# Performance work log

Hardware: AMD Instinct MI355X
Metric: run time of the kernel (lower is better)

## Reference

```python
import jax, jax.numpy as jnp
import numpy as np

D_MODEL = 512
N_HEADS = 8
D_HEAD = D_MODEL // N_HEADS
SCALE = 1.0 / np.sqrt(D_MODEL).astype(np.float32)  # source divides by sqrt(d_model), not sqrt(d_head)


def setup_inputs() -> dict:
    key = jax.random.key(0)
    ks = jax.random.split(key, 9)
    B, S = 4, 2048
    std = 1.0 / np.sqrt(D_MODEL).astype(np.float32)
    x = jax.random.normal(ks[0], (B, S, D_MODEL), dtype=jnp.float32)
    Wq = jax.random.normal(ks[1], (D_MODEL, D_MODEL), dtype=jnp.float32) * std
    bq = jnp.zeros((D_MODEL,), jnp.float32)
    Wk = jax.random.normal(ks[2], (D_MODEL, D_MODEL), dtype=jnp.float32) * std
    bk = jnp.zeros((D_MODEL,), jnp.float32)
    Wv = jax.random.normal(ks[3], (D_MODEL, D_MODEL), dtype=jnp.float32) * std
    bv = jnp.zeros((D_MODEL,), jnp.float32)
    Wo = jax.random.normal(ks[4], (D_MODEL, D_MODEL), dtype=jnp.float32) * std
    bo = jnp.zeros((D_MODEL,), jnp.float32)
    return {"x": x, "Wq": Wq, "bq": bq, "Wk": Wk, "bk": bk,
            "Wv": Wv, "bv": bv, "Wo": Wo, "bo": bo}


def reference(x, Wq, bq, Wk, bk, Wv, bv, Wo, bo):
    B, S, _ = x.shape
    # projections -> [B, H, S, Dh]
    def split_heads(t):
        return t.reshape(B, S, N_HEADS, D_HEAD).transpose(0, 2, 1, 3)
    q = split_heads(x @ Wq + bq)
    k = split_heads(x @ Wk + bk)
    v = split_heads(x @ Wv + bv)
    # scores: [B, H, S, S], scaled by 1/sqrt(d_model) as in source
    scores = jnp.einsum('bhqd,bhkd->bhqk', q, k) * SCALE
    weights = jax.nn.softmax(scores, axis=-1)
    # dropout is identity at inference time
    att = jnp.einsum('bhqk,bhkd->bhqd', weights, v)
    att = att.transpose(0, 2, 1, 3).reshape(B, S, D_MODEL)
    return att @ Wo + bo
```

## Files before the change

kernel.cpp:

```cpp
#include <hip/hip_runtime.h>
#include <math.h>

#define BATCH   4
#define S_LEN   2048
#define DMODEL  512
#define NHEADS  8
#define DHEAD   64
#define M_TOT   8192
#define ATT_SCALE 0.04419417382415922f
#define QSCALE (ATT_SCALE * 1.44269504088896f)

using short8  = __attribute__((ext_vector_type(8))) short;
using short4v = __attribute__((ext_vector_type(4))) short;
using floatx4 = __attribute__((ext_vector_type(4))) float;

__device__ __forceinline__ ushort f2bf(float f) {
    union { float f; unsigned u; } x; x.f = f;
    unsigned u = x.u + 0x7FFFu + ((x.u >> 16) & 1u);
    return (ushort)(u >> 16);
}
__device__ __forceinline__ unsigned pk2(float a, float b) {
    return (unsigned)f2bf(a) | ((unsigned)f2bf(b) << 16);
}
__device__ __forceinline__ unsigned pkr2(float a, float b) {
    unsigned ua = __float_as_uint(a) + 0x8000u;
    unsigned ub = __float_as_uint(b) + 0x8000u;
    return __builtin_amdgcn_perm(ub, ua, 0x07060302u);
}

__global__ __launch_bounds__(256) void prep(
    const float* __restrict__ x,
    const float* __restrict__ Wq, const float* __restrict__ Wk,
    const float* __restrict__ Wv, const float* __restrict__ Wo,
    ushort* __restrict__ xb, ushort* __restrict__ WT)
{
    const int bid = blockIdx.x;
    if (bid < 4096) {
        const int i = (bid * 256 + threadIdx.x) * 4;
        float4 f = *(const float4*)(x + i);
        uint2 o; o.x = pk2(f.x, f.y); o.y = pk2(f.z, f.w);
        *(uint2*)(xb + i) = o;
    } else {
        const int rb = bid - 4096;
        const int p  = rb >> 6;
        const int rem = rb & 63;
        const int n  = (rem >> 5) * 256 + threadIdx.x;
        const int k0 = (rem & 31) * 16;
        const float* W = (p == 0) ? Wq : (p == 1) ? Wk : (p == 2) ? Wv : Wo;
        unsigned u[8];
        #pragma unroll
        for (int j = 0; j < 8; ++j) {
            float a = W[(k0 + 2 * j)     * DMODEL + n];
            float b = W[(k0 + 2 * j + 1) * DMODEL + n];
            u[j] = pk2(a, b);
        }
        ushort* dst = WT + ((size_t)p * DMODEL + n) * DMODEL + k0;
        *(uint4*)dst       = *(uint4*)&u[0];
        *(uint4*)(dst + 8) = *(uint4*)&u[4];
    }
}

__global__ __launch_bounds__(256, 4) void qkv_gemm(
    const ushort* __restrict__ xb, const ushort* __restrict__ WT,
    const float* __restrict__ bq, const float* __restrict__ bk, const float* __restrict__ bv,
    ushort* __restrict__ q, ushort* __restrict__ k, ushort* __restrict__ vT)
{
    __shared__ ushort SMEM[128 * 136];
    ushort (*A)[40] = (ushort(*)[40])SMEM;
    ushort (*B)[40] = (ushort(*)[40])(SMEM + 128 * 40);
    ushort (*CT)[136] = (ushort(*)[136])SMEM;

    const int tid = threadIdx.x;
    const int wv  = tid >> 6, lane = tid & 63, l16 = lane & 15, quad = lane >> 4;
    const int m0  = blockIdx.x * 128;
    const int ng0 = blockIdx.y * 128;
    const int p   = ng0 >> 9;
    const int n0  = ng0 & 511;
    const ushort* Wp  = WT + (size_t)p * DMODEL * DMODEL + (size_t)n0 * DMODEL;
    const float* bias = (p == 0) ? bq : (p == 1) ? bk : bv;
    const float scl   = (p == 0) ? QSCALE : 1.0f;

    const int wm = (wv & 1) * 64, wn = (wv >> 1) * 64;
    floatx4 acc[4][4] = {};
    const int ar = tid >> 1, ac = (tid & 1) * 16;

    uint4 pa0, pa1, pb0, pb1;
    pa0 = *(const uint4*)(xb + (size_t)(m0 + ar) * DMODEL + ac);
    pa1 = *(const uint4*)(xb + (size_t)(m0 + ar) * DMODEL + ac + 8);
    pb0 = *(const uint4*)(Wp + (size_t)ar * DMODEL + ac);
    pb1 = *(const uint4*)(Wp + (size_t)ar * DMODEL + ac + 8);

    for (int k0 = 0; k0 < DMODEL; k0 += 32) {
        *(uint4*)&A[ar][ac] = pa0; *(uint4*)&A[ar][ac + 8] = pa1;
        *(uint4*)&B[ar][ac] = pb0; *(uint4*)&B[ar][ac + 8] = pb1;
        __syncthreads();

        if (k0 + 32 < DMODEL) {
            pa0 = *(const uint4*)(xb + (size_t)(m0 + ar) * DMODEL + k0 + 32 + ac);
            pa1 = *(const uint4*)(xb + (size_t)(m0 + ar) * DMODEL + k0 + 32 + ac + 8);
            pb0 = *(const uint4*)(Wp + (size_t)ar * DMODEL + k0 + 32 + ac);
            pb1 = *(const uint4*)(Wp + (size_t)ar * DMODEL + k0 + 32 + ac + 8);
        }

        short8 af[4], bf[4];
        #pragma unroll
        for (int i = 0; i < 4; ++i) af[i] = *(const short8*)&A[wm + i * 16 + l16][quad * 8];
        #pragma unroll
        for (int c = 0; c < 4; ++c) bf[c] = *(const short8*)&B[wn + c * 16 + l16][quad * 8];
        #pragma unroll
        for (int i = 0; i < 4; ++i)
            #pragma unroll
            for (int c = 0; c < 4; ++c)
                acc[i][c] = __builtin_amdgcn_mfma_f32_16x16x32_bf16(af[i], bf[c], acc[i][c], 0, 0, 0);
        __syncthreads();
    }

    if (p < 2) {
        #pragma unroll
        for (int c = 0; c < 4; ++c) {
            const int n = n0 + wn + c * 16 + l16;
            const float bb = bias[n];
            const int h = n >> 6, dh = n & 63;
            #pragma unroll
            for (int i = 0; i < 4; ++i)
                #pragma unroll
                for (int r = 0; r < 4; ++r) {
                    const int m = m0 + wm + i * 16 + quad * 4 + r;
                    const int b = m >> 11, s = m & 2047;
                    const ushort val = f2bf((acc[i][c][r] + bb) * scl);
                    if (p == 0) q[((size_t)(b * NHEADS + h) * S_LEN + s) * DHEAD + dh] = val;
                    else        k[((size_t)(b * NHEADS + h) * S_LEN + s) * DHEAD + dh] = val;
                }
        }
    } else {
        #pragma unroll
        for (int c = 0; c < 4; ++c) {
            const int n = wn + c * 16 + l16;
            const float bb = bias[n0 + n];
            #pragma unroll
            for (int i = 0; i < 4; ++i) {
                uint2 o;
                o.x = pk2(acc[i][c][0] + bb, acc[i][c][1] + bb);
                o.y = pk2(acc[i][c][2] + bb, acc[i][c][3] + bb);
                *(uint2*)&CT[n][wm + i * 16 + quad * 4] = o;
            }
        }
        __syncthreads();
        const int n  = tid >> 1, mh = (tid & 1) * 64;
        const int gn = n0 + n;
        const int h  = gn >> 6, dh = gn & 63;
        const int b  = m0 >> 11, sb = (m0 & 2047) + mh;
        ushort* dst = vT + ((size_t)(b * NHEADS + h) * DHEAD + dh) * S_LEN + sb;
        #pragma unroll
        for (int j = 0; j < 8; ++j)
            *(uint4*)(dst + j * 8) = *(const uint4*)&CT[n][mh + j * 8];
    }
}

__global__ __launch_bounds__(256, 4) void attn(
    const ushort* __restrict__ Q, const ushort* __restrict__ K,
    const ushort* __restrict__ vT,
    float* __restrict__ Opart, float* __restrict__ Lpart, const int KT)
{
    __shared__ ushort Klds[2][64][72];
    __shared__ ushort Vt[2][64][72];

    const int tid = threadIdx.x;
    const int wv  = tid >> 6, lane = tid & 63, l16 = lane & 15, quad = lane >> 4;
    const int q0  = blockIdx.x * 128;
    const int bh  = blockIdx.y;
    const int ck  = blockIdx.z;
    const int kbase = ck * KT;
    const ushort* Qh = Q  + (size_t)bh * S_LEN * DHEAD;
    const ushort* Kh = K  + (size_t)bh * S_LEN * DHEAD;
    const ushort* Vh = vT + (size_t)bh * DHEAD * S_LEN;

    short8 qf[2][2];
    #pragma unroll
    for (int ni = 0; ni < 2; ++ni) {
        const ushort* qrow = Qh + (size_t)(q0 + wv * 32 + ni * 16 + l16) * DHEAD;
        qf[0][ni] = *(const short8*)(qrow + quad * 8);
        qf[1][ni] = *(const short8*)(qrow + 32 + quad * 8);
    }

    floatx4 oacc[4][2] = {};
    float lsum[2] = {0.f, 0.f};

    const int srow = tid >> 2, sc0 = (tid & 3) * 16;
    uint4 ka, kb, va, vb;
    {
        const ushort* Ks = Kh + (size_t)(kbase * 64 + srow) * DHEAD + sc0;
        const ushort* Vs = Vh + (size_t)srow * S_LEN + kbase * 64 + sc0;
        ka = *(const uint4*)Ks; kb = *(const uint4*)(Ks + 8);
        va = *(const uint4*)Vs; vb = *(const uint4*)(Vs + 8);
    }

    for (int kt = 0; kt < KT; ++kt) {
        const int buf = kt & 1;
        *(uint4*)&Klds[buf][srow][sc0] = ka; *(uint4*)&Klds[buf][srow][sc0 + 8] = kb;
        *(uint4*)&Vt[buf][srow][sc0]   = va; *(uint4*)&Vt[buf][srow][sc0 + 8]   = vb;
        __syncthreads();

        if (kt + 1 < KT) {
            const ushort* Ks = Kh + (size_t)((kbase + kt + 1) * 64 + srow) * DHEAD + sc0;
            const ushort* Vs = Vh + (size_t)srow * S_LEN + (kbase + kt + 1) * 64 + sc0;
            ka = *(const uint4*)Ks; kb = *(const uint4*)(Ks + 8);
            va = *(const uint4*)Vs; vb = *(const uint4*)(Vs + 8);
        }

        #pragma unroll
        for (int mi = 0; mi < 4; ++mi) {
            floatx4 s0 = {}, s1 = {};
            #pragma unroll
            for (int s = 0; s < 2; ++s) {
                short8 kf = *(const short8*)&Klds[buf][mi * 16 + l16][s * 32 + quad * 8];
                s0 = __builtin_amdgcn_mfma_f32_16x16x32_bf16(kf, qf[s][0], s0, 0, 0, 0);
                s1 = __builtin_amdgcn_mfma_f32_16x16x32_bf16(kf, qf[s][1], s1, 0, 0, 0);
            }
            short4v vfr[4];
            #pragma unroll
            for (int c = 0; c < 4; ++c)
                vfr[c] = *(const short4v*)&Vt[buf][c * 16 + l16][mi * 16 + quad * 4];

            {
                const float p0 = __builtin_amdgcn_exp2f(s0[0]);
                const float p1 = __builtin_amdgcn_exp2f(s0[1]);
                const float p2 = __builtin_amdgcn_exp2f(s0[2]);
                const float p3 = __builtin_amdgcn_exp2f(s0[3]);
                lsum[0] += (p0 + p1) + (p2 + p3);
                uint2 o; o.x = pkr2(p0, p1); o.y = pkr2(p2, p3);
                short4v pf; *(uint2*)&pf = o;
                #pragma unroll
                for (int c = 0; c < 4; ++c)
                    oacc[c][0] = __builtin_amdgcn_mfma_f32_16x16x16bf16_1k(vfr[c], pf, oacc[c][0], 0, 0, 0);
            }
            {
                const float p0 = __builtin_amdgcn_exp2f(s1[0]);
                const float p1 = __builtin_amdgcn_exp2f(s1[1]);
                const float p2 = __builtin_amdgcn_exp2f(s1[2]);
                const float p3 = __builtin_amdgcn_exp2f(s1[3]);
                lsum[1] += (p0 + p1) + (p2 + p3);
                uint2 o; o.x = pkr2(p0, p1); o.y = pkr2(p2, p3);
                short4v pf; *(uint2*)&pf = o;
                #pragma unroll
                for (int c = 0; c < 4; ++c)
                    oacc[c][1] = __builtin_amdgcn_mfma_f32_16x16x16bf16_1k(vfr[c], pf, oacc[c][1], 0, 0, 0);
            }
        }
    }

    float tot[2];
    #pragma unroll
    for (int ni = 0; ni < 2; ++ni) {
        float t = lsum[ni];
        t += __shfl_xor(t, 16, 64);
        t += __shfl_xor(t, 32, 64);
        tot[ni] = t;
    }

    #pragma unroll
    for (int ni = 0; ni < 2; ++ni) {
        const int qi = q0 + wv * 32 + ni * 16 + l16;
        const size_t row = (size_t)(ck * 32 + bh) * S_LEN + qi;
        if (quad == 0) Lpart[row] = tot[ni];
        #pragma unroll
        for (int mi = 0; mi < 4; ++mi) {
            float4 o = { oacc[mi][ni][0], oacc[mi][ni][1],
                         oacc[mi][ni][2], oacc[mi][ni][3] };
            *(float4*)&Opart[row * DHEAD + mi * 16 + quad * 4] = o;
        }
    }
}

__global__ __launch_bounds__(256, 4) void out_gemm(
    const float* __restrict__ Opart, const float* __restrict__ Lpart,
    const ushort* __restrict__ WoT, const float* __restrict__ bo,
    float* __restrict__ out)
{
    __shared__ ushort A[64][40];
    __shared__ ushort B[128][40];

    const int tid = threadIdx.x;
    const int wv  = tid >> 6, lane = tid & 63, l16 = lane & 15, quad = lane >> 4;
    const int m0 = blockIdx.x * 64;
    const int n0 = blockIdx.y * 128;

    const int ar = tid >> 2, ac = (tid & 3) * 8;
    const int am = m0 + ar, ab = am >> 11, aq = am & 2047;
    float invl[NHEADS];
    #pragma unroll
    for (int h = 0; h < NHEADS; ++h) {
        const size_t rw = (size_t)(ab * NHEADS + h) * S_LEN + aq;
        invl[h] = 1.f / (Lpart[rw] + Lpart[65536 + rw]);
    }
    const int br = tid >> 1, bc = (tid & 1) * 16;

    floatx4 acc[8] = {};

    for (int k0 = 0; k0 < DMODEL; k0 += 32) {
        const int kk = k0 + ac, h = kk >> 6, dh = kk & 63;
        const float* p0 = Opart + ((size_t)(ab * NHEADS + h) * S_LEN + aq) * DHEAD + dh;
        const float* p1 = p0 + (size_t)65536 * DHEAD;
        float4 a0 = *(const float4*)p0,       a1 = *(const float4*)(p0 + 4);
        float4 c0 = *(const float4*)p1,       c1 = *(const float4*)(p1 + 4);
        const float iv = invl[h];
        uint2 u0, u1;
        u0.x = pk2((a0.x + c0.x) * iv, (a0.y + c0.y) * iv);
        u0.y = pk2((a0.z + c0.z) * iv, (a0.w + c0.w) * iv);
        u1.x = pk2((a1.x + c1.x) * iv, (a1.y + c1.y) * iv);
        u1.y = pk2((a1.z + c1.z) * iv, (a1.w + c1.w) * iv);
        *(uint2*)&A[ar][ac]     = u0;
        *(uint2*)&A[ar][ac + 4] = u1;

        uint4 b0 = *(const uint4*)(WoT + (size_t)(n0 + br) * DMODEL + k0 + bc);
        uint4 b1 = *(const uint4*)(WoT + (size_t)(n0 + br) * DMODEL + k0 + bc + 8);
        *(uint4*)&B[br][bc] = b0; *(uint4*)&B[br][bc + 8] = b1;
        __syncthreads();

        short8 af = *(const short8*)&A[wv * 16 + l16][quad * 8];
        #pragma unroll
        for (int c = 0; c < 8; ++c) {
            short8 bf = *(const short8*)&B[c * 16 + l16][quad * 8];
            acc[c] = __builtin_amdgcn_mfma_f32_16x16x32_bf16(af, bf, acc[c], 0, 0, 0);
        }
        __syncthreads();
    }

    #pragma unroll
    for (int c = 0; c < 8; ++c) {
        const int n = n0 + c * 16 + l16;
        const float bb = bo[n];
        #pragma unroll
        for (int r = 0; r < 4; ++r) {
            const int m = m0 + wv * 16 + quad * 4 + r;
            out[(size_t)m * DMODEL + n] = acc[c][r] + bb;
        }
    }
}

extern "C" void kernel_launch(void* const* d_in, const int* in_sizes, int n_in,
                              void* d_out, int out_size, void* d_ws, size_t ws_size,
                              hipStream_t stream)
{
    const float* x  = (const float*)d_in[0];
    const float* Wq = (const float*)d_in[1];
    const float* bq = (const float*)d_in[2];
    const float* Wk = (const float*)d_in[3];
    const float* bk = (const float*)d_in[4];
    const float* Wv = (const float*)d_in[5];
    const float* bv = (const float*)d_in[6];
    const float* Wo = (const float*)d_in[7];
    const float* bo = (const float*)d_in[8];
    float* out = (float*)d_out;

    ushort* ws = (ushort*)d_ws;
    const size_t SZ = (size_t)M_TOT * DMODEL;
    ushort* xb  = ws;
    ushort* WT  = ws + SZ;
    ushort* q   = WT + 4 * (size_t)DMODEL * DMODEL;
    ushort* k   = q + SZ;
    ushort* vT  = k + SZ;
    float*  Opart = (float*)(vT + SZ);
    float*  Lpart = Opart + 2 * (size_t)32 * S_LEN * DHEAD;

    prep<<<4096 + 256, 256, 0, stream>>>(x, Wq, Wk, Wv, Wo, xb, WT);

    qkv_gemm<<<dim3(M_TOT / 128, 3 * DMODEL / 128), 256, 0, stream>>>(
        xb, WT, bq, bk, bv, q, k, vT);

    attn<<<dim3(S_LEN / 128, BATCH * NHEADS, 2), 256, 0, stream>>>(
        q, k, vT, Opart, Lpart, S_LEN / 64 / 2);

    out_gemm<<<dim3(M_TOT / 64, DMODEL / 128), 256, 0, stream>>>(
        Opart, Lpart, WT + 3 * (size_t)DMODEL * DMODEL, bo, out);
}
```

Measured before the change: 177.5 us.

## Remap attention blocks XCD-aware and prefetch K/V two tiles ahead

```diff
diff --git a/kernel.cpp b/kernel.cpp
--- a/kernel.cpp
+++ b/kernel.cpp
@@ -167,10 +167,18 @@
 
     const int tid = threadIdx.x;
     const int wv  = tid >> 6, lane = tid & 63, l16 = lane & 15, quad = lane >> 4;
-    const int q0  = blockIdx.x * 128;
-    const int bh  = blockIdx.y;
-    const int ck  = blockIdx.z;
+
+    const int bid = blockIdx.x;
+    const int xg   = bid & 7;
+    const int rest = bid >> 3;
+    const int qt   = rest & 15;
+    const int gh   = rest >> 4;
+    const int g    = gh * 8 + xg;
+    const int bh   = g >> 1;
+    const int ck   = g & 1;
+    const int q0   = qt * 128;
     const int kbase = ck * KT;
+
     const ushort* Qh = Q  + (size_t)bh * S_LEN * DHEAD;
     const ushort* Kh = K  + (size_t)bh * S_LEN * DHEAD;
     const ushort* Vh = vT + (size_t)bh * DHEAD * S_LEN;
@@ -187,25 +195,26 @@
     float lsum[2] = {0.f, 0.f};
 
     const int srow = tid >> 2, sc0 = (tid & 3) * 16;
-    uint4 ka, kb, va, vb;
-    {
-        const ushort* Ks = Kh + (size_t)(kbase * 64 + srow) * DHEAD + sc0;
-        const ushort* Vs = Vh + (size_t)srow * S_LEN + kbase * 64 + sc0;
-        ka = *(const uint4*)Ks; kb = *(const uint4*)(Ks + 8);
-        va = *(const uint4*)Vs; vb = *(const uint4*)(Vs + 8);
+    uint4 ka[2], kb[2], va[2], vb[2];
+    #pragma unroll
+    for (int t = 0; t < 2; ++t) {
+        const ushort* Ks = Kh + (size_t)((kbase + t) * 64 + srow) * DHEAD + sc0;
+        const ushort* Vs = Vh + (size_t)srow * S_LEN + (kbase + t) * 64 + sc0;
+        ka[t] = *(const uint4*)Ks; kb[t] = *(const uint4*)(Ks + 8);
+        va[t] = *(const uint4*)Vs; vb[t] = *(const uint4*)(Vs + 8);
     }
 
     for (int kt = 0; kt < KT; ++kt) {
         const int buf = kt & 1;
-        *(uint4*)&Klds[buf][srow][sc0] = ka; *(uint4*)&Klds[buf][srow][sc0 + 8] = kb;
-        *(uint4*)&Vt[buf][srow][sc0]   = va; *(uint4*)&Vt[buf][srow][sc0 + 8]   = vb;
-        __syncthreads();
-
-        if (kt + 1 < KT) {
-            const ushort* Ks = Kh + (size_t)((kbase + kt + 1) * 64 + srow) * DHEAD + sc0;
-            const ushort* Vs = Vh + (size_t)srow * S_LEN + (kbase + kt + 1) * 64 + sc0;
-            ka = *(const uint4*)Ks; kb = *(const uint4*)(Ks + 8);
-            va = *(const uint4*)Vs; vb = *(const uint4*)(Vs + 8);
+        *(uint4*)&Klds[buf][srow][sc0] = ka[buf]; *(uint4*)&Klds[buf][srow][sc0 + 8] = kb[buf];
+        *(uint4*)&Vt[buf][srow][sc0]   = va[buf]; *(uint4*)&Vt[buf][srow][sc0 + 8]   = vb[buf];
+        __syncthreads();
+
+        if (kt + 2 < KT) {
+            const ushort* Ks = Kh + (size_t)((kbase + kt + 2) * 64 + srow) * DHEAD + sc0;
+            const ushort* Vs = Vh + (size_t)srow * S_LEN + (kbase + kt + 2) * 64 + sc0;
+            ka[buf] = *(const uint4*)Ks; kb[buf] = *(const uint4*)(Ks + 8);
+            va[buf] = *(const uint4*)Vs; vb[buf] = *(const uint4*)(Vs + 8);
         }
 
         #pragma unroll
@@ -368,8 +377,7 @@
     qkv_gemm<<<dim3(M_TOT / 128, 3 * DMODEL / 128), 256, 0, stream>>>(
         xb, WT, bq, bk, bv, q, k, vT);
 
-    attn<<<dim3(S_LEN / 128, BATCH * NHEADS, 2), 256, 0, stream>>>(
-        q, k, vT, Opart, Lpart, S_LEN / 64 / 2);
+    attn<<<1024, 256, 0, stream>>>(q, k, vT, Opart, Lpart, S_LEN / 64 / 2);
 
     out_gemm<<<dim3(M_TOT / 64, DMODEL / 128), 256, 0, stream>>>(
         Opart, Lpart, WT + 3 * (size_t)DMODEL * DMODEL, bo, out);
```

Result: slower. 218.5 us (+23.1%).

## Fuse x bf16 conversion into QKV GEMM loads and remap attention grid to XCDs

Applied to the files above, without the earlier changes.

```diff
diff --git a/kernel.cpp b/kernel.cpp
--- a/kernel.cpp
+++ b/kernel.cpp
@@ -29,39 +29,30 @@
 }
 
 __global__ __launch_bounds__(256) void prep(
-    const float* __restrict__ x,
     const float* __restrict__ Wq, const float* __restrict__ Wk,
     const float* __restrict__ Wv, const float* __restrict__ Wo,
-    ushort* __restrict__ xb, ushort* __restrict__ WT)
-{
-    const int bid = blockIdx.x;
-    if (bid < 4096) {
-        const int i = (bid * 256 + threadIdx.x) * 4;
-        float4 f = *(const float4*)(x + i);
-        uint2 o; o.x = pk2(f.x, f.y); o.y = pk2(f.z, f.w);
-        *(uint2*)(xb + i) = o;
-    } else {
-        const int rb = bid - 4096;
-        const int p  = rb >> 6;
-        const int rem = rb & 63;
-        const int n  = (rem >> 5) * 256 + threadIdx.x;
-        const int k0 = (rem & 31) * 16;
-        const float* W = (p == 0) ? Wq : (p == 1) ? Wk : (p == 2) ? Wv : Wo;
-        unsigned u[8];
-        #pragma unroll
-        for (int j = 0; j < 8; ++j) {
-            float a = W[(k0 + 2 * j)     * DMODEL + n];
-            float b = W[(k0 + 2 * j + 1) * DMODEL + n];
-            u[j] = pk2(a, b);
-        }
-        ushort* dst = WT + ((size_t)p * DMODEL + n) * DMODEL + k0;
-        *(uint4*)dst       = *(uint4*)&u[0];
-        *(uint4*)(dst + 8) = *(uint4*)&u[4];
-    }
+    ushort* __restrict__ WT)
+{
+    const int rb = blockIdx.x;
+    const int p  = rb >> 6;
+    const int rem = rb & 63;
+    const int n  = (rem >> 5) * 256 + threadIdx.x;
+    const int k0 = (rem & 31) * 16;
+    const float* W = (p == 0) ? Wq : (p == 1) ? Wk : (p == 2) ? Wv : Wo;
+    unsigned u[8];
+    #pragma unroll
+    for (int j = 0; j < 8; ++j) {
+        float a = W[(k0 + 2 * j)     * DMODEL + n];
+        float b = W[(k0 + 2 * j + 1) * DMODEL + n];
+        u[j] = pk2(a, b);
+    }
+    ushort* dst = WT + ((size_t)p * DMODEL + n) * DMODEL + k0;
+    *(uint4*)dst       = *(uint4*)&u[0];
+    *(uint4*)(dst + 8) = *(uint4*)&u[4];
 }
 
 __global__ __launch_bounds__(256, 4) void qkv_gemm(
-    const ushort* __restrict__ xb, const ushort* __restrict__ WT,
+    const float* __restrict__ x, const ushort* __restrict__ WT,
     const float* __restrict__ bq, const float* __restrict__ bk, const float* __restrict__ bv,
     ushort* __restrict__ q, ushort* __restrict__ k, ushort* __restrict__ vT)
 {
@@ -83,10 +74,19 @@
     const int wm = (wv & 1) * 64, wn = (wv >> 1) * 64;
     floatx4 acc[4][4] = {};
     const int ar = tid >> 1, ac = (tid & 1) * 16;
+    const float* xrow = x + (size_t)(m0 + ar) * DMODEL;
 
     uint4 pa0, pa1, pb0, pb1;
-    pa0 = *(const uint4*)(xb + (size_t)(m0 + ar) * DMODEL + ac);
-    pa1 = *(const uint4*)(xb + (size_t)(m0 + ar) * DMODEL + ac + 8);
+    {
+        float4 f0 = *(const float4*)(xrow + ac);
+        float4 f1 = *(const float4*)(xrow + ac + 4);
+        float4 f2 = *(const float4*)(xrow + ac + 8);
+        float4 f3 = *(const float4*)(xrow + ac + 12);
+        pa0.x = pk2(f0.x, f0.y); pa0.y = pk2(f0.z, f0.w);
+        pa0.z = pk2(f1.x, f1.y); pa0.w = pk2(f1.z, f1.w);
+        pa1.x = pk2(f2.x, f2.y); pa1.y = pk2(f2.z, f2.w);
+        pa1.z = pk2(f3.x, f3.y); pa1.w = pk2(f3.z, f3.w);
+    }
     pb0 = *(const uint4*)(Wp + (size_t)ar * DMODEL + ac);
     pb1 = *(const uint4*)(Wp + (size_t)ar * DMODEL + ac + 8);
 
@@ -96,8 +96,14 @@
         __syncthreads();
 
         if (k0 + 32 < DMODEL) {
-            pa0 = *(const uint4*)(xb + (size_t)(m0 + ar) * DMODEL + k0 + 32 + ac);
-            pa1 = *(const uint4*)(xb + (size_t)(m0 + ar) * DMODEL + k0 + 32 + ac + 8);
+            float4 f0 = *(const float4*)(xrow + k0 + 32 + ac);
+            float4 f1 = *(const float4*)(xrow + k0 + 32 + ac + 4);
+            float4 f2 = *(const float4*)(xrow + k0 + 32 + ac + 8);
+            float4 f3 = *(const float4*)(xrow + k0 + 32 + ac + 12);
+            pa0.x = pk2(f0.x, f0.y); pa0.y = pk2(f0.z, f0.w);
+            pa0.z = pk2(f1.x, f1.y); pa0.w = pk2(f1.z, f1.w);
+            pa1.x = pk2(f2.x, f2.y); pa1.y = pk2(f2.z, f2.w);
+            pa1.z = pk2(f3.x, f3.y); pa1.w = pk2(f3.z, f3.w);
             pb0 = *(const uint4*)(Wp + (size_t)ar * DMODEL + k0 + 32 + ac);
             pb1 = *(const uint4*)(Wp + (size_t)ar * DMODEL + k0 + 32 + ac + 8);
         }
@@ -167,10 +173,18 @@
 
     const int tid = threadIdx.x;
     const int wv  = tid >> 6, lane = tid & 63, l16 = lane & 15, quad = lane >> 4;
-    const int q0  = blockIdx.x * 128;
-    const int bh  = blockIdx.y;
-    const int ck  = blockIdx.z;
+
+    const int bid = blockIdx.x;
+    const int xg   = bid & 7;
+    const int rest = bid >> 3;
+    const int qt   = rest & 15;
+    const int gh   = rest >> 4;
+    const int g    = gh * 8 + xg;
+    const int bh   = g >> 1;
+    const int ck   = g & 1;
+    const int q0   = qt * 128;
     const int kbase = ck * KT;
+
     const ushort* Qh = Q  + (size_t)bh * S_LEN * DHEAD;
     const ushort* Kh = K  + (size_t)bh * S_LEN * DHEAD;
     const ushort* Vh = vT + (size_t)bh * DHEAD * S_LEN;
@@ -355,21 +369,19 @@
 
     ushort* ws = (ushort*)d_ws;
     const size_t SZ = (size_t)M_TOT * DMODEL;
-    ushort* xb  = ws;
-    ushort* WT  = ws + SZ;
+    ushort* WT  = ws;
     ushort* q   = WT + 4 * (size_t)DMODEL * DMODEL;
     ushort* k   = q + SZ;
     ushort* vT  = k + SZ;
     float*  Opart = (float*)(vT + SZ);
     float*  Lpart = Opart + 2 * (size_t)32 * S_LEN * DHEAD;
 
-    prep<<<4096 + 256, 256, 0, stream>>>(x, Wq, Wk, Wv, Wo, xb, WT);
+    prep<<<256, 256, 0, stream>>>(Wq, Wk, Wv, Wo, WT);
 
     qkv_gemm<<<dim3(M_TOT / 128, 3 * DMODEL / 128), 256, 0, stream>>>(
-        xb, WT, bq, bk, bv, q, k, vT);
-
-    attn<<<dim3(S_LEN / 128, BATCH * NHEADS, 2), 256, 0, stream>>>(
-        q, k, vT, Opart, Lpart, S_LEN / 64 / 2);
+        x, WT, bq, bk, bv, q, k, vT);
+
+    attn<<<1024, 256, 0, stream>>>(q, k, vT, Opart, Lpart, S_LEN / 64 / 2);
 
     out_gemm<<<dim3(M_TOT / 64, DMODEL / 128), 256, 0, stream>>>(
         Opart, Lpart, WT + 3 * (size_t)DMODEL * DMODEL, bo, out);
```

Result: no change. 179.1 us (+0.9%).

## Coalesce Q/K epilogue via LDS staging and remap attention blocks for XCD locality

Applied to the files above, without the earlier changes.

```diff
diff --git a/kernel.cpp b/kernel.cpp
--- a/kernel.cpp
+++ b/kernel.cpp
@@ -68,7 +68,7 @@
     __shared__ ushort SMEM[128 * 136];
     ushort (*A)[40] = (ushort(*)[40])SMEM;
     ushort (*B)[40] = (ushort(*)[40])(SMEM + 128 * 40);
-    ushort (*CT)[136] = (ushort(*)[136])SMEM;
+    ushort (*CC)[136] = (ushort(*)[136])SMEM;
 
     const int tid = threadIdx.x;
     const int wv  = tid >> 6, lane = tid & 63, l16 = lane & 15, quad = lane >> 4;
@@ -90,49 +90,73 @@
     pb0 = *(const uint4*)(Wp + (size_t)ar * DMODEL + ac);
     pb1 = *(const uint4*)(Wp + (size_t)ar * DMODEL + ac + 8);
 
-    for (int k0 = 0; k0 < DMODEL; k0 += 32) {
-        *(uint4*)&A[ar][ac] = pa0; *(uint4*)&A[ar][ac + 8] = pa1;
-        *(uint4*)&B[ar][ac] = pb0; *(uint4*)&B[ar][ac + 8] = pb1;
-        __syncthreads();
-
-        if (k0 + 32 < DMODEL) {
-            pa0 = *(const uint4*)(xb + (size_t)(m0 + ar) * DMODEL + k0 + 32 + ac);
-            pa1 = *(const uint4*)(xb + (size_t)(m0 + ar) * DMODEL + k0 + 32 + ac + 8);
-            pb0 = *(const uint4*)(Wp + (size_t)ar * DMODEL + k0 + 32 + ac);
-            pb1 = *(const uint4*)(Wp + (size_t)ar * DMODEL + k0 + 32 + ac + 8);
-        }
-
-        short8 af[4], bf[4];
-        #pragma unroll
-        for (int i = 0; i < 4; ++i) af[i] = *(const short8*)&A[wm + i * 16 + l16][quad * 8];
-        #pragma unroll
-        for (int c = 0; c < 4; ++c) bf[c] = *(const short8*)&B[wn + c * 16 + l16][quad * 8];
-        #pragma unroll
-        for (int i = 0; i < 4; ++i)
-            #pragma unroll
-            for (int c = 0; c < 4; ++c)
-                acc[i][c] = __builtin_amdgcn_mfma_f32_16x16x32_bf16(af[i], bf[c], acc[i][c], 0, 0, 0);
-        __syncthreads();
-    }
-
     if (p < 2) {
-        #pragma unroll
-        for (int c = 0; c < 4; ++c) {
-            const int n = n0 + wn + c * 16 + l16;
-            const float bb = bias[n];
-            const int h = n >> 6, dh = n & 63;
+        for (int k0 = 0; k0 < DMODEL; k0 += 32) {
+            *(uint4*)&A[ar][ac] = pa0; *(uint4*)&A[ar][ac + 8] = pa1;
+            *(uint4*)&B[ar][ac] = pb0; *(uint4*)&B[ar][ac + 8] = pb1;
+            __syncthreads();
+            if (k0 + 32 < DMODEL) {
+                pa0 = *(const uint4*)(xb + (size_t)(m0 + ar) * DMODEL + k0 + 32 + ac);
+                pa1 = *(const uint4*)(xb + (size_t)(m0 + ar) * DMODEL + k0 + 32 + ac + 8);
+                pb0 = *(const uint4*)(Wp + (size_t)ar * DMODEL + k0 + 32 + ac);
+                pb1 = *(const uint4*)(Wp + (size_t)ar * DMODEL + k0 + 32 + ac + 8);
+            }
+            short8 af[4], bf[4];
+            #pragma unroll
+            for (int i = 0; i < 4; ++i) af[i] = *(const short8*)&A[wm + i * 16 + l16][quad * 8];
+            #pragma unroll
+            for (int c = 0; c < 4; ++c) bf[c] = *(const short8*)&B[wn + c * 16 + l16][quad * 8];
             #pragma unroll
             for (int i = 0; i < 4; ++i)
                 #pragma unroll
-                for (int r = 0; r < 4; ++r) {
-                    const int m = m0 + wm + i * 16 + quad * 4 + r;
-                    const int b = m >> 11, s = m & 2047;
-                    const ushort val = f2bf((acc[i][c][r] + bb) * scl);
-                    if (p == 0) q[((size_t)(b * NHEADS + h) * S_LEN + s) * DHEAD + dh] = val;
-                    else        k[((size_t)(b * NHEADS + h) * S_LEN + s) * DHEAD + dh] = val;
-                }
-        }
+                for (int c = 0; c < 4; ++c)
+                    acc[c][i] = __builtin_amdgcn_mfma_f32_16x16x32_bf16(bf[c], af[i], acc[c][i], 0, 0, 0);
+            __syncthreads();
+        }
+        #pragma unroll
+        for (int c = 0; c < 4; ++c) {
+            const int nl = wn + c * 16 + quad * 4;
+            float4 bb = *(const float4*)&bias[n0 + nl];
+            #pragma unroll
+            for (int i = 0; i < 4; ++i) {
+                uint2 o;
+                o.x = pk2((acc[c][i][0] + bb.x) * scl, (acc[c][i][1] + bb.y) * scl);
+                o.y = pk2((acc[c][i][2] + bb.z) * scl, (acc[c][i][3] + bb.w) * scl);
+                *(uint2*)&CC[wm + i * 16 + l16][nl] = o;
+            }
+        }
+        __syncthreads();
+        const int m  = m0 + (tid >> 1);
+        const int nh = (tid & 1) * 64;
+        const int b  = m >> 11, s = m & 2047;
+        const int h  = (n0 + nh) >> 6;
+        ushort* dst = ((p == 0) ? q : k) + ((size_t)(b * NHEADS + h) * S_LEN + s) * DHEAD;
+        #pragma unroll
+        for (int j = 0; j < 8; ++j)
+            *(uint4*)(dst + j * 8) = *(const uint4*)&CC[tid >> 1][nh + j * 8];
     } else {
+        for (int k0 = 0; k0 < DMODEL; k0 += 32) {
+            *(uint4*)&A[ar][ac] = pa0; *(uint4*)&A[ar][ac + 8] = pa1;
+            *(uint4*)&B[ar][ac] = pb0; *(uint4*)&B[ar][ac + 8] = pb1;
+            __syncthreads();
+            if (k0 + 32 < DMODEL) {
+                pa0 = *(const uint4*)(xb + (size_t)(m0 + ar) * DMODEL + k0 + 32 + ac);
+                pa1 = *(const uint4*)(xb + (size_t)(m0 + ar) * DMODEL + k0 + 32 + ac + 8);
+                pb0 = *(const uint4*)(Wp + (size_t)ar * DMODEL + k0 + 32 + ac);
+                pb1 = *(const uint4*)(Wp + (size_t)ar * DMODEL + k0 + 32 + ac + 8);
+            }
+            short8 af[4], bf[4];
+            #pragma unroll
+            for (int i = 0; i < 4; ++i) af[i] = *(const short8*)&A[wm + i * 16 + l16][quad * 8];
+            #pragma unroll
+            for (int c = 0; c < 4; ++c) bf[c] = *(const short8*)&B[wn + c * 16 + l16][quad * 8];
+            #pragma unroll
+            for (int i = 0; i < 4; ++i)
+                #pragma unroll
+                for (int c = 0; c < 4; ++c)
+                    acc[i][c] = __builtin_amdgcn_mfma_f32_16x16x32_bf16(af[i], bf[c], acc[i][c], 0, 0, 0);
+            __syncthreads();
+        }
         #pragma unroll
         for (int c = 0; c < 4; ++c) {
             const int n = wn + c * 16 + l16;
@@ -142,7 +166,7 @@
                 uint2 o;
                 o.x = pk2(acc[i][c][0] + bb, acc[i][c][1] + bb);
                 o.y = pk2(acc[i][c][2] + bb, acc[i][c][3] + bb);
-                *(uint2*)&CT[n][wm + i * 16 + quad * 4] = o;
+                *(uint2*)&CC[n][wm + i * 16 + quad * 4] = o;
             }
         }
         __syncthreads();
@@ -153,7 +177,7 @@
         ushort* dst = vT + ((size_t)(b * NHEADS + h) * DHEAD + dh) * S_LEN + sb;
         #pragma unroll
         for (int j = 0; j < 8; ++j)
-            *(uint4*)(dst + j * 8) = *(const uint4*)&CT[n][mh + j * 8];
+            *(uint4*)(dst + j * 8) = *(const uint4*)&CC[n][mh + j * 8];
     }
 }
 
@@ -167,10 +191,18 @@
 
     const int tid = threadIdx.x;
     const int wv  = tid >> 6, lane = tid & 63, l16 = lane & 15, quad = lane >> 4;
-    const int q0  = blockIdx.x * 128;
-    const int bh  = blockIdx.y;
-    const int ck  = blockIdx.z;
+
+    const int bid = blockIdx.x;
+    const int xg   = bid & 7;
+    const int rest = bid >> 3;
+    const int qt   = rest & 15;
+    const int gh   = rest >> 4;
+    const int g    = gh * 8 + xg;
+    const int bh   = g >> 1;
+    const int ck   = g & 1;
+    const int q0   = qt * 128;
     const int kbase = ck * KT;
+
     const ushort* Qh = Q  + (size_t)bh * S_LEN * DHEAD;
     const ushort* Kh = K  + (size_t)bh * S_LEN * DHEAD;
     const ushort* Vh = vT + (size_t)bh * DHEAD * S_LEN;
@@ -368,8 +400,7 @@
     qkv_gemm<<<dim3(M_TOT / 128, 3 * DMODEL / 128), 256, 0, stream>>>(
         xb, WT, bq, bk, bv, q, k, vT);
 
-    attn<<<dim3(S_LEN / 128, BATCH * NHEADS, 2), 256, 0, stream>>>(
-        q, k, vT, Opart, Lpart, S_LEN / 64 / 2);
+    attn<<<1024, 256, 0, stream>>>(q, k, vT, Opart, Lpart, S_LEN / 64 / 2);
 
     out_gemm<<<dim3(M_TOT / 64, DMODEL / 128), 256, 0, stream>>>(
         Opart, Lpart, WT + 3 * (size_t)DMODEL * DMODEL, bo, out);
```

After: 182.0 us. 1.03x slower.
